# Performance work log

Hardware: AMD Instinct MI355X
Metric: run time of the kernel (lower is better)

Reference implementation:

```python
import jax, jax.numpy as jnp
import numpy as np

N_NODES = 50000
D_IN = 64
HID = 64
OUT = 64
NEG_SLOPE = 0.2


def setup_inputs() -> dict:
    key = jax.random.key(0)
    ks = jax.random.split(key, 16)
    s = 1.0 / np.sqrt(D_IN)
    inp = {
        "x": jax.random.normal(ks[0], (N_NODES, D_IN), dtype=jnp.float32),
        "edge_index": jax.random.randint(ks[1], (2, 1200000), 0, N_NODES, dtype=jnp.int64),
        # conv1 (GATConv, heads=1): separate src/dst projections + attention vectors + bias
        "W1_src": jax.random.uniform(ks[2], (D_IN, HID), jnp.float32, -s, s),
        "W1_dst": jax.random.uniform(ks[3], (D_IN, HID), jnp.float32, -s, s),
        "att1_src": jax.random.uniform(ks[4], (HID,), jnp.float32, -s, s),
        "att1_dst": jax.random.uniform(ks[5], (HID,), jnp.float32, -s, s),
        "b1": jnp.zeros((HID,), jnp.float32),
        # lin1 residual
        "Wl1": jax.random.uniform(ks[6], (D_IN, HID), jnp.float32, -s, s),
        "bl1": jnp.zeros((HID,), jnp.float32),
        # conv2
        "W2_src": jax.random.uniform(ks[7], (HID, OUT), jnp.float32, -s, s),
        "W2_dst": jax.random.uniform(ks[8], (HID, OUT), jnp.float32, -s, s),
        "att2_src": jax.random.uniform(ks[9], (OUT,), jnp.float32, -s, s),
        "att2_dst": jax.random.uniform(ks[10], (OUT,), jnp.float32, -s, s),
        "b2": jnp.zeros((OUT,), jnp.float32),
        # lin2 residual
        "Wl2": jax.random.uniform(ks[11], (HID, OUT), jnp.float32, -s, s),
        "bl2": jnp.zeros((OUT,), jnp.float32),
    }
    return inp


def _gat_conv(x, W_src, W_dst, att_src, att_dst, bias, src, dst, n_nodes):
    # project nodes: [N, C]
    h_src = x @ W_src
    h_dst = x @ W_dst
    # per-node attention logits: [N]
    a_src = h_src @ att_src
    a_dst = h_dst @ att_dst
    # per-edge score, leaky relu (slope 0.2)
    e = a_src[src] + a_dst[dst]  # [E]
    e = jnp.where(e >= 0, e, NEG_SLOPE * e)
    # segment softmax over incoming edges of each dst node
    seg_max = jax.lax.stop_gradient(
        jax.ops.segment_max(e, dst, num_segments=n_nodes))  # [N]
    w = jnp.exp(e - seg_max[dst])  # [E]
    seg_sum = jax.ops.segment_sum(w, dst, num_segments=n_nodes)  # [N]
    alpha = w / seg_sum[dst]  # [E]
    # weighted scatter-add of gathered src features
    msg = h_src[src] * alpha[:, None]  # [E, C]
    out = jax.ops.segment_sum(msg, dst, num_segments=n_nodes)  # [N, C]
    return out + bias


def reference(x, edge_index, W1_src, W1_dst, att1_src, att1_dst, b1, Wl1, bl1,
              W2_src, W2_dst, att2_src, att2_dst, b2, Wl2, bl2):
    src, dst = edge_index[0], edge_index[1]
    n = x.shape[0]
    h = _gat_conv(x, W1_src, W1_dst, att1_src, att1_dst, b1, src, dst, n)
    h = jax.nn.relu(h + x @ Wl1 + bl1)
    o = _gat_conv(h, W2_src, W2_dst, att2_src, att2_dst, b2, src, dst, n)
    o = jax.nn.relu(o + h @ Wl2 + bl2)
    return o
```

## Files before the change

### kernel.cpp

```cpp
#include <hip/hip_runtime.h>
#include <hip/hip_fp16.h>

#define NEG 0.2f
#define BSHIFT 9
#define BNODES 512
#define ECAP 14336

__global__ __launch_bounds__(256) void bin_prep(
    const int* __restrict__ src, const int* __restrict__ dst,
    int* __restrict__ gcur, unsigned* __restrict__ binned, int E, int K,
    const float* __restrict__ W1s, const float* __restrict__ a1s,
    const float* __restrict__ W1d, const float* __restrict__ a1d,
    const float* __restrict__ W2s, const float* __restrict__ a2s,
    const float* __restrict__ W2d, const float* __restrict__ a2d,
    float* __restrict__ vecs) {
    int t = threadIdx.x;
    if (blockIdx.x == gridDim.x - 1) {
        int g = t >> 6, k = t & 63;
        const float* W = (g == 0) ? W1s : (g == 1) ? W1d : (g == 2) ? W2s : W2d;
        const float* a = (g == 0) ? a1s : (g == 1) ? a1d : (g == 2) ? a2s : a2d;
        float s = 0.f;
        #pragma unroll 8
        for (int j = 0; j < 64; ++j) s += W[k * 64 + j] * a[j];
        vecs[t] = s;
        return;
    }
    __shared__ int h[128], cbase[128], cur[128];
    if (t < 128) h[t] = 0;
    __syncthreads();
    int base = blockIdx.x * 2048;
    #pragma unroll
    for (int i = 0; i < 8; ++i) {
        int idx = base + i * 256 + t;
        if (idx < E) atomicAdd(&h[dst[idx] >> BSHIFT], 1);
    }
    __syncthreads();
    if (t < K) {
        cbase[t] = t * ECAP + (h[t] ? atomicAdd(&gcur[t], h[t]) : 0);
        cur[t] = 0;
    }
    __syncthreads();
    #pragma unroll
    for (int i = 0; i < 8; ++i) {
        int idx = base + i * 256 + t;
        if (idx < E) {
            int d = dst[idx], s = src[idx];
            int b = d >> BSHIFT;
            int pos = cbase[b] + atomicAdd(&cur[b], 1);
            binned[pos] = ((unsigned)s << BSHIFT) | (unsigned)(d & (BNODES - 1));
        }
    }
}

__global__ __launch_bounds__(256) void csr_gemm(
    const unsigned* __restrict__ binned, int* __restrict__ ssrc,
    const int* __restrict__ gcur, int* __restrict__ rowbeg, int* __restrict__ rowend,
    const float* __restrict__ x, const float* __restrict__ Wsrc,
    const float* __restrict__ Wl, const float* __restrict__ vsrc,
    const float* __restrict__ vdst, const float* __restrict__ bconv,
    const float* __restrict__ blin,
    __half2* __restrict__ hsrc, float* __restrict__ base_out,
    float* __restrict__ asrc, float* __restrict__ adst, int N, int K) {
    __shared__ union {
        struct { __half WsH[4096]; __half WlH[4096]; float xs[64 * 65];
                 float bias[64]; float vs[64]; float vd[64]; } g;
        struct { int lh[BNODES]; int ps[256]; } c;
    } sm;
    int tid = threadIdx.x;
    int blk = blockIdx.x;

    if (blk < K) {
        int base = blk * ECAP;
        int cnt = min(gcur[blk], ECAP);
        sm.c.lh[tid] = 0; sm.c.lh[tid + 256] = 0;
        __syncthreads();
        for (int i = tid; i < cnt; i += 256)
            atomicAdd(&sm.c.lh[binned[base + i] & (BNODES - 1)], 1);
        __syncthreads();
        int a0 = sm.c.lh[2 * tid], a1 = sm.c.lh[2 * tid + 1];
        sm.c.ps[tid] = a0 + a1;
        __syncthreads();
        for (int off = 1; off < 256; off <<= 1) {
            int v = (tid >= off) ? sm.c.ps[tid - off] : 0;
            __syncthreads();
            sm.c.ps[tid] += v;
            __syncthreads();
        }
        int exc = sm.c.ps[tid] - (a0 + a1);
        int node0 = blk * BNODES + 2 * tid, node1 = node0 + 1;
        if (node0 < N) { rowbeg[node0] = base + exc;      rowend[node0] = base + exc + a0; }
        if (node1 < N) { rowbeg[node1] = base + exc + a0; rowend[node1] = base + exc + a0 + a1; }
        __syncthreads();
        sm.c.lh[2 * tid] = exc; sm.c.lh[2 * tid + 1] = exc + a0;
        __syncthreads();
        for (int i = tid; i < cnt; i += 256) {
            unsigned e = binned[base + i];
            int pos = atomicAdd(&sm.c.lh[e & (BNODES - 1)], 1);
            ssrc[base + pos] = (int)(e >> BSHIFT);
        }
        return;
    }

    int gb = blk - K;
    #pragma unroll
    for (int i = 0; i < 4; ++i) {
        int idx4 = tid * 4 + i * 1024;
        float4 ws = *(const float4*)&Wsrc[idx4];
        float4 wl = *(const float4*)&Wl[idx4];
        *(__half2*)&sm.g.WsH[idx4]     = __floats2half2_rn(ws.x, ws.y);
        *(__half2*)&sm.g.WsH[idx4 + 2] = __floats2half2_rn(ws.z, ws.w);
        *(__half2*)&sm.g.WlH[idx4]     = __floats2half2_rn(wl.x, wl.y);
        *(__half2*)&sm.g.WlH[idx4 + 2] = __floats2half2_rn(wl.z, wl.w);
    }
    if (tid < 64) {
        sm.g.bias[tid] = bconv[tid] + blin[tid];
        sm.g.vs[tid]   = vsrc[tid];
        sm.g.vd[tid]   = vdst[tid];
    }
    int row0 = gb * 64;
    int rows = min(64, N - row0);
    #pragma unroll
    for (int i = 0; i < 16; ++i) {
        int idx = tid + i * 256;
        int r = idx >> 6, cc = idx & 63;
        if (r < rows) sm.g.xs[r * 65 + cc] = x[(size_t)(row0 + r) * 64 + cc];
    }
    __syncthreads();

    int r0 = (tid >> 3) * 2;
    int cg = tid & 7, c0 = cg * 8;
    if (r0 >= rows) return;

    float a0[8], a1[8], b0[8], b1[8];
    #pragma unroll
    for (int i = 0; i < 8; ++i) { a0[i] = a1[i] = b0[i] = b1[i] = 0.f; }
    float as0 = 0.f, ad0 = 0.f, as1 = 0.f, ad1 = 0.f;

    #pragma unroll 8
    for (int k = 0; k < 64; ++k) {
        float xv0 = sm.g.xs[r0 * 65 + k];
        float xv1 = sm.g.xs[(r0 + 1) * 65 + k];
        float4 wsv = *(const float4*)&sm.g.WsH[(k << 6) + c0];
        float4 wlv = *(const float4*)&sm.g.WlH[(k << 6) + c0];
        const __half2* hs = (const __half2*)&wsv;
        const __half2* hl = (const __half2*)&wlv;
        #pragma unroll
        for (int p = 0; p < 4; ++p) {
            float2 w = __half22float2(hs[p]);
            a0[2*p]   += xv0 * w.x;  a0[2*p+1] += xv0 * w.y;
            a1[2*p]   += xv1 * w.x;  a1[2*p+1] += xv1 * w.y;
            float2 l = __half22float2(hl[p]);
            b0[2*p]   += xv0 * l.x;  b0[2*p+1] += xv0 * l.y;
            b1[2*p]   += xv1 * l.x;  b1[2*p+1] += xv1 * l.y;
        }
        float vsk = sm.g.vs[k], vdk = sm.g.vd[k];
        as0 += xv0 * vsk;  ad0 += xv0 * vdk;
        as1 += xv1 * vsk;  ad1 += xv1 * vdk;
    }

    int rg0 = row0 + r0, rg1 = rg0 + 1;
    bool row1ok = (r0 + 1) < rows;
    float4 pack;
    ((__half2*)&pack)[0] = __floats2half2_rn(a0[0], a0[1]);
    ((__half2*)&pack)[1] = __floats2half2_rn(a0[2], a0[3]);
    ((__half2*)&pack)[2] = __floats2half2_rn(a0[4], a0[5]);
    ((__half2*)&pack)[3] = __floats2half2_rn(a0[6], a0[7]);
    *(float4*)&hsrc[(size_t)rg0 * 32 + (c0 >> 1)] = pack;
    if (row1ok) {
        ((__half2*)&pack)[0] = __floats2half2_rn(a1[0], a1[1]);
        ((__half2*)&pack)[1] = __floats2half2_rn(a1[2], a1[3]);
        ((__half2*)&pack)[2] = __floats2half2_rn(a1[4], a1[5]);
        ((__half2*)&pack)[3] = __floats2half2_rn(a1[6], a1[7]);
        *(float4*)&hsrc[(size_t)rg1 * 32 + (c0 >> 1)] = pack;
    }
    float4 bA = *(const float4*)&sm.g.bias[c0];
    float4 bB = *(const float4*)&sm.g.bias[c0 + 4];
    float4 o;
    o.x = b0[0] + bA.x; o.y = b0[1] + bA.y; o.z = b0[2] + bA.z; o.w = b0[3] + bA.w;
    *(float4*)&base_out[(size_t)rg0 * 64 + c0] = o;
    o.x = b0[4] + bB.x; o.y = b0[5] + bB.y; o.z = b0[6] + bB.z; o.w = b0[7] + bB.w;
    *(float4*)&base_out[(size_t)rg0 * 64 + c0 + 4] = o;
    if (row1ok) {
        o.x = b1[0] + bA.x; o.y = b1[1] + bA.y; o.z = b1[2] + bA.z; o.w = b1[3] + bA.w;
        *(float4*)&base_out[(size_t)rg1 * 64 + c0] = o;
        o.x = b1[4] + bB.x; o.y = b1[5] + bB.y; o.z = b1[6] + bB.z; o.w = b1[7] + bB.w;
        *(float4*)&base_out[(size_t)rg1 * 64 + c0 + 4] = o;
    }
    if (cg == 0) {
        asrc[rg0] = as0; adst[rg0] = ad0;
        if (row1ok) { asrc[rg1] = as1; adst[rg1] = ad1; }
    }
}

__global__ __launch_bounds__(256) void node_gemm(
    const float* __restrict__ x, const float* __restrict__ Wsrc,
    const float* __restrict__ Wl, const float* __restrict__ vsrc,
    const float* __restrict__ vdst, const float* __restrict__ bconv,
    const float* __restrict__ blin,
    __half2* __restrict__ hsrc, float* __restrict__ base_out,
    float* __restrict__ asrc, float* __restrict__ adst, int n) {
    __shared__ __half WsH[4096];
    __shared__ __half WlH[4096];
    __shared__ float xs[64 * 65];
    __shared__ float bias_s[64], vs_s[64], vd_s[64];

    int tid = threadIdx.x;
    #pragma unroll
    for (int i = 0; i < 4; ++i) {
        int idx4 = tid * 4 + i * 1024;
        float4 ws = *(const float4*)&Wsrc[idx4];
        float4 wl = *(const float4*)&Wl[idx4];
        *(__half2*)&WsH[idx4]     = __floats2half2_rn(ws.x, ws.y);
        *(__half2*)&WsH[idx4 + 2] = __floats2half2_rn(ws.z, ws.w);
        *(__half2*)&WlH[idx4]     = __floats2half2_rn(wl.x, wl.y);
        *(__half2*)&WlH[idx4 + 2] = __floats2half2_rn(wl.z, wl.w);
    }
    if (tid < 64) {
        bias_s[tid] = bconv[tid] + blin[tid];
        vs_s[tid]   = vsrc[tid];
        vd_s[tid]   = vdst[tid];
    }
    int row0 = blockIdx.x * 64;
    int rows = min(64, n - row0);
    #pragma unroll
    for (int i = 0; i < 16; ++i) {
        int idx = tid + i * 256;
        int r = idx >> 6, cc = idx & 63;
        if (r < rows) xs[r * 65 + cc] = x[(size_t)(row0 + r) * 64 + cc];
    }
    __syncthreads();

    int r0 = (tid >> 3) * 2;
    int cg = tid & 7, c0 = cg * 8;
    if (r0 >= rows) return;

    float a0[8], a1[8], b0[8], b1[8];
    #pragma unroll
    for (int i = 0; i < 8; ++i) { a0[i] = a1[i] = b0[i] = b1[i] = 0.f; }
    float as0 = 0.f, ad0 = 0.f, as1 = 0.f, ad1 = 0.f;

    #pragma unroll 8
    for (int k = 0; k < 64; ++k) {
        float xv0 = xs[r0 * 65 + k];
        float xv1 = xs[(r0 + 1) * 65 + k];
        float4 wsv = *(const float4*)&WsH[(k << 6) + c0];
        float4 wlv = *(const float4*)&WlH[(k << 6) + c0];
        const __half2* hs = (const __half2*)&wsv;
        const __half2* hl = (const __half2*)&wlv;
        #pragma unroll
        for (int p = 0; p < 4; ++p) {
            float2 w = __half22float2(hs[p]);
            a0[2*p]   += xv0 * w.x;  a0[2*p+1] += xv0 * w.y;
            a1[2*p]   += xv1 * w.x;  a1[2*p+1] += xv1 * w.y;
            float2 l = __half22float2(hl[p]);
            b0[2*p]   += xv0 * l.x;  b0[2*p+1] += xv0 * l.y;
            b1[2*p]   += xv1 * l.x;  b1[2*p+1] += xv1 * l.y;
        }
        float vsk = vs_s[k], vdk = vd_s[k];
        as0 += xv0 * vsk;  ad0 += xv0 * vdk;
        as1 += xv1 * vsk;  ad1 += xv1 * vdk;
    }

    int rg0 = row0 + r0, rg1 = rg0 + 1;
    bool row1ok = (r0 + 1) < rows;
    float4 pack;
    ((__half2*)&pack)[0] = __floats2half2_rn(a0[0], a0[1]);
    ((__half2*)&pack)[1] = __floats2half2_rn(a0[2], a0[3]);
    ((__half2*)&pack)[2] = __floats2half2_rn(a0[4], a0[5]);
    ((__half2*)&pack)[3] = __floats2half2_rn(a0[6], a0[7]);
    *(float4*)&hsrc[(size_t)rg0 * 32 + (c0 >> 1)] = pack;
    if (row1ok) {
        ((__half2*)&pack)[0] = __floats2half2_rn(a1[0], a1[1]);
        ((__half2*)&pack)[1] = __floats2half2_rn(a1[2], a1[3]);
        ((__half2*)&pack)[2] = __floats2half2_rn(a1[4], a1[5]);
        ((__half2*)&pack)[3] = __floats2half2_rn(a1[6], a1[7]);
        *(float4*)&hsrc[(size_t)rg1 * 32 + (c0 >> 1)] = pack;
    }
    float4 bA = *(const float4*)&bias_s[c0];
    float4 bB = *(const float4*)&bias_s[c0 + 4];
    float4 o;
    o.x = b0[0] + bA.x; o.y = b0[1] + bA.y; o.z = b0[2] + bA.z; o.w = b0[3] + bA.w;
    *(float4*)&base_out[(size_t)rg0 * 64 + c0] = o;
    o.x = b0[4] + bB.x; o.y = b0[5] + bB.y; o.z = b0[6] + bB.z; o.w = b0[7] + bB.w;
    *(float4*)&base_out[(size_t)rg0 * 64 + c0 + 4] = o;
    if (row1ok) {
        o.x = b1[0] + bA.x; o.y = b1[1] + bA.y; o.z = b1[2] + bA.z; o.w = b1[3] + bA.w;
        *(float4*)&base_out[(size_t)rg1 * 64 + c0] = o;
        o.x = b1[4] + bB.x; o.y = b1[5] + bB.y; o.z = b1[6] + bB.z; o.w = b1[7] + bB.w;
        *(float4*)&base_out[(size_t)rg1 * 64 + c0 + 4] = o;
    }
    if (cg == 0) {
        asrc[rg0] = as0; adst[rg0] = ad0;
        if (row1ok) { asrc[rg1] = as1; adst[rg1] = ad1; }
    }
}

__global__ __launch_bounds__(256) void gat_aggregate(
    const int* __restrict__ rowbeg, const int* __restrict__ rowend,
    const int* __restrict__ ssrc,
    const float* __restrict__ asrc, const float* __restrict__ adst,
    const __half2* __restrict__ hsrc, const float* __restrict__ base,
    float* __restrict__ out, int N) {
    int d = blockIdx.x * 4 + (threadIdx.x >> 6);
    int lane = threadIdx.x & 63;
    int half_id = lane >> 5;
    int c2 = lane & 31;
    if (d >= N) return;
    int beg = rowbeg[d], end = rowend[d];
    float ad = adst[d];
    float sumw = 0.f, accx = 0.f, accy = 0.f;

    while (beg < end) {
        int nb = min(64, end - beg);
        int s_l = 0; float w_l = 0.f;
        if (lane < nb) {
            s_l = ssrc[beg + lane];
            float e = asrc[s_l] + ad;
            e = (e >= 0.f) ? e : NEG * e;
            w_l = __expf(e);
        }
        int i = 0;
        for (; i + 7 < nb; i += 8) {
            int i0 = i + half_id, i1 = i + 2 + half_id;
            int i2 = i + 4 + half_id, i3 = i + 6 + half_id;
            int   s0 = __shfl(s_l, i0, 64), s1 = __shfl(s_l, i1, 64);
            int   s2 = __shfl(s_l, i2, 64), s3 = __shfl(s_l, i3, 64);
            float w0 = __shfl(w_l, i0, 64), w1 = __shfl(w_l, i1, 64);
            float w2 = __shfl(w_l, i2, 64), w3 = __shfl(w_l, i3, 64);
            float2 h0 = __half22float2(hsrc[(size_t)s0 * 32 + c2]);
            float2 h1 = __half22float2(hsrc[(size_t)s1 * 32 + c2]);
            float2 h2 = __half22float2(hsrc[(size_t)s2 * 32 + c2]);
            float2 h3 = __half22float2(hsrc[(size_t)s3 * 32 + c2]);
            sumw += (w0 + w1) + (w2 + w3);
            accx += w0 * h0.x + w1 * h1.x + w2 * h2.x + w3 * h3.x;
            accy += w0 * h0.y + w1 * h1.y + w2 * h2.y + w3 * h3.y;
        }
        for (; i + 3 < nb; i += 4) {
            int i0 = i + half_id, i1 = i + 2 + half_id;
            int   s0 = __shfl(s_l, i0, 64), s1 = __shfl(s_l, i1, 64);
            float w0 = __shfl(w_l, i0, 64), w1 = __shfl(w_l, i1, 64);
            float2 h0 = __half22float2(hsrc[(size_t)s0 * 32 + c2]);
            float2 h1 = __half22float2(hsrc[(size_t)s1 * 32 + c2]);
            sumw += w0 + w1;
            accx += w0 * h0.x + w1 * h1.x;
            accy += w0 * h0.y + w1 * h1.y;
        }
        for (; i < nb; i += 2) {
            int idx = i + half_id;
            int   s = __shfl(s_l, idx, 64);
            float w = __shfl(w_l, idx, 64);
            float2 h = __half22float2(hsrc[(size_t)s * 32 + c2]);
            sumw += w;
            accx += w * h.x;
            accy += w * h.y;
        }
        beg += nb;
    }
    accx += __shfl_xor(accx, 32, 64);
    accy += __shfl_xor(accy, 32, 64);
    sumw += __shfl_xor(sumw, 32, 64);

    if (half_id == 0) {
        float2 b2 = *(const float2*)&base[(size_t)d * 64 + 2 * c2];
        float invw = (sumw > 0.f) ? 1.f / sumw : 0.f;
        float2 o;
        o.x = fmaxf(b2.x + accx * invw, 0.f);
        o.y = fmaxf(b2.y + accy * invw, 0.f);
        *(float2*)&out[(size_t)d * 64 + 2 * c2] = o;
    }
}

extern "C" void kernel_launch(void* const* d_in, const int* in_sizes, int n_in,
                              void* d_out, int out_size, void* d_ws, size_t ws_size,
                              hipStream_t stream) {
    const float* x    = (const float*)d_in[0];
    const int*   ei   = (const int*)d_in[1];
    const float* W1s  = (const float*)d_in[2];
    const float* W1d  = (const float*)d_in[3];
    const float* a1s  = (const float*)d_in[4];
    const float* a1d  = (const float*)d_in[5];
    const float* b1   = (const float*)d_in[6];
    const float* Wl1  = (const float*)d_in[7];
    const float* bl1  = (const float*)d_in[8];
    const float* W2s  = (const float*)d_in[9];
    const float* W2d  = (const float*)d_in[10];
    const float* a2s  = (const float*)d_in[11];
    const float* a2d  = (const float*)d_in[12];
    const float* b2   = (const float*)d_in[13];
    const float* Wl2  = (const float*)d_in[14];
    const float* bl2  = (const float*)d_in[15];

    const int N = in_sizes[0] / 64;
    const int E = in_sizes[1] / 2;
    const int* src = ei;
    const int* dst = ei + E;
    const int K = (N + BNODES - 1) >> BSHIFT;

    float* ws = (float*)d_ws;
    size_t o = 0;
    __half2* hsrcH = (__half2*)(ws + o); o += (size_t)N * 32;
    float* base   = ws + o; o += (size_t)N * 64;
    float* asrc   = ws + o; o += N;
    float* adst   = ws + o; o += N;
    float* vecs   = ws + o; o += 256;
    int* rowbeg = (int*)(ws + o); o += N;
    int* rowend = (int*)(ws + o); o += N;
    int* gcur   = (int*)(ws + o); o += 128;
    unsigned* binned = (unsigned*)(ws + o); o += (size_t)K * ECAP;
    int* ssrc   = (int*)(ws + o); o += (size_t)K * ECAP;

    float* hmid = (float*)d_out;

    const int EB = (E + 2047) / 2048;

    hipMemsetAsync(gcur, 0, 128 * sizeof(int), stream);
    bin_prep<<<EB + 1, 256, 0, stream>>>(src, dst, gcur, binned, E, K,
                                         W1s, a1s, W1d, a1d, W2s, a2s, W2d, a2d, vecs);

    csr_gemm<<<K + (N + 63) / 64, 256, 0, stream>>>(
        binned, ssrc, gcur, rowbeg, rowend,
        x, W1s, Wl1, vecs, vecs + 64, b1, bl1,
        hsrcH, base, asrc, adst, N, K);

    gat_aggregate<<<(N + 3) / 4, 256, 0, stream>>>(rowbeg, rowend, ssrc, asrc, adst,
                                                   hsrcH, base, hmid, N);

    node_gemm<<<(N + 63) / 64, 256, 0, stream>>>(hmid, W2s, Wl2, vecs + 128, vecs + 192,
                                                 b2, bl2, hsrcH, base, asrc, adst, N);
    gat_aggregate<<<(N + 3) / 4, 256, 0, stream>>>(rowbeg, rowend, ssrc, asrc, adst,
                                                   hsrcH, base, (float*)d_out, N);
}
```

Baseline: 240.0 us.

## Fuse layer-1 aggregation into layer-2 GEMM and widen aggregation gathers

Adds an agg_gemm kernel in which each block aggregates 64 destination nodes of layer 1 directly into shared memory, then runs the layer-2 projection GEMM on that tile. This removes the hmid round trip through global memory and one kernel launch. Separate hsrc and asrc/adst buffers per layer keep layer-2 writes from clobbering layer-1 inputs that other blocks still read. Aggregation is reorganised so 16 lanes each gather 8 bytes, handling 4 edges per step instead of 2. The trade-off is less parallelism in the fused aggregation, since each wave walks 16 nodes in sequence and the larger shared-memory footprint may lower occupancy.

```diff
diff --git a/kernel.cpp b/kernel.cpp
--- a/kernel.cpp
+++ b/kernel.cpp
@@ -5,6 +5,58 @@
 #define BSHIFT 9
 #define BNODES 512
 #define ECAP 14336
+
+__device__ __forceinline__ void agg_core(
+    int beg, int end, float ad, int lane, int g, int l,
+    const int* __restrict__ ssrc, const float* __restrict__ asrc,
+    const float2* __restrict__ h8,
+    float& a0, float& a1, float& a2, float& a3, float& sumw) {
+    a0 = a1 = a2 = a3 = sumw = 0.f;
+    while (beg < end) {
+        int nb = min(64, end - beg);
+        int s_l = 0; float w_l = 0.f;
+        if (lane < nb) {
+            s_l = ssrc[beg + lane];
+            float e = asrc[s_l] + ad;
+            e = (e >= 0.f) ? e : NEG * e;
+            w_l = __expf(e);
+        }
+        int i = 0;
+        for (; i + 7 < nb; i += 8) {
+            int iA = i + g, iB = i + 4 + g;
+            int   sA = __shfl(s_l, iA, 64), sB = __shfl(s_l, iB, 64);
+            float wA = __shfl(w_l, iA, 64), wB = __shfl(w_l, iB, 64);
+            float2 rA = h8[(size_t)sA * 16 + l];
+            float2 rB = h8[(size_t)sB * 16 + l];
+            float2 fA0 = __half22float2(((const __half2*)&rA)[0]);
+            float2 fA1 = __half22float2(((const __half2*)&rA)[1]);
+            float2 fB0 = __half22float2(((const __half2*)&rB)[0]);
+            float2 fB1 = __half22float2(((const __half2*)&rB)[1]);
+            sumw += wA + wB;
+            a0 += wA * fA0.x + wB * fB0.x;
+            a1 += wA * fA0.y + wB * fB0.y;
+            a2 += wA * fA1.x + wB * fB1.x;
+            a3 += wA * fA1.y + wB * fB1.y;
+        }
+        for (; i < nb; i += 4) {
+            int iA = i + g;
+            int   sA = __shfl(s_l, iA, 64);
+            float wA = __shfl(w_l, iA, 64);
+            float2 rA = h8[(size_t)sA * 16 + l];
+            float2 fA0 = __half22float2(((const __half2*)&rA)[0]);
+            float2 fA1 = __half22float2(((const __half2*)&rA)[1]);
+            sumw += wA;
+            a0 += wA * fA0.x; a1 += wA * fA0.y;
+            a2 += wA * fA1.x; a3 += wA * fA1.y;
+        }
+        beg += nb;
+    }
+    a0 += __shfl_xor(a0, 16, 64); a0 += __shfl_xor(a0, 32, 64);
+    a1 += __shfl_xor(a1, 16, 64); a1 += __shfl_xor(a1, 32, 64);
+    a2 += __shfl_xor(a2, 16, 64); a2 += __shfl_xor(a2, 32, 64);
+    a3 += __shfl_xor(a3, 16, 64); a3 += __shfl_xor(a3, 32, 64);
+    sumw += __shfl_xor(sumw, 16, 64); sumw += __shfl_xor(sumw, 32, 64);
+}
 
 __global__ __launch_bounds__(256) void bin_prep(
     const int* __restrict__ src, const int* __restrict__ dst,
@@ -52,6 +104,77 @@
     }
 }
 
+__device__ __forceinline__ void gemm_tile(
+    int tid, int row0, int rows,
+    const __half* WsH, const __half* WlH, const float* xs,
+    const float* bias_s, const float* vs_s, const float* vd_s,
+    __half2* __restrict__ hsrc, float* __restrict__ base_out,
+    float* __restrict__ asrc, float* __restrict__ adst) {
+    int r0 = (tid >> 3) * 2;
+    int cg = tid & 7, c0 = cg * 8;
+    if (r0 >= rows) return;
+
+    float a0[8], a1[8], b0[8], b1[8];
+    #pragma unroll
+    for (int i = 0; i < 8; ++i) { a0[i] = a1[i] = b0[i] = b1[i] = 0.f; }
+    float as0 = 0.f, ad0 = 0.f, as1 = 0.f, ad1 = 0.f;
+
+    #pragma unroll 8
+    for (int k = 0; k < 64; ++k) {
+        float xv0 = xs[r0 * 65 + k];
+        float xv1 = xs[(r0 + 1) * 65 + k];
+        float4 wsv = *(const float4*)&WsH[(k << 6) + c0];
+        float4 wlv = *(const float4*)&WlH[(k << 6) + c0];
+        const __half2* hs = (const __half2*)&wsv;
+        const __half2* hl = (const __half2*)&wlv;
+        #pragma unroll
+        for (int p = 0; p < 4; ++p) {
+            float2 w = __half22float2(hs[p]);
+            a0[2*p]   += xv0 * w.x;  a0[2*p+1] += xv0 * w.y;
+            a1[2*p]   += xv1 * w.x;  a1[2*p+1] += xv1 * w.y;
+            float2 l = __half22float2(hl[p]);
+            b0[2*p]   += xv0 * l.x;  b0[2*p+1] += xv0 * l.y;
+            b1[2*p]   += xv1 * l.x;  b1[2*p+1] += xv1 * l.y;
+        }
+        float vsk = vs_s[k], vdk = vd_s[k];
+        as0 += xv0 * vsk;  ad0 += xv0 * vdk;
+        as1 += xv1 * vsk;  ad1 += xv1 * vdk;
+    }
+
+    int rg0 = row0 + r0, rg1 = rg0 + 1;
+    bool row1ok = (r0 + 1) < rows;
+    float4 pack;
+    ((__half2*)&pack)[0] = __floats2half2_rn(a0[0], a0[1]);
+    ((__half2*)&pack)[1] = __floats2half2_rn(a0[2], a0[3]);
+    ((__half2*)&pack)[2] = __floats2half2_rn(a0[4], a0[5]);
+    ((__half2*)&pack)[3] = __floats2half2_rn(a0[6], a0[7]);
+    *(float4*)&hsrc[(size_t)rg0 * 32 + (c0 >> 1)] = pack;
+    if (row1ok) {
+        ((__half2*)&pack)[0] = __floats2half2_rn(a1[0], a1[1]);
+        ((__half2*)&pack)[1] = __floats2half2_rn(a1[2], a1[3]);
+        ((__half2*)&pack)[2] = __floats2half2_rn(a1[4], a1[5]);
+        ((__half2*)&pack)[3] = __floats2half2_rn(a1[6], a1[7]);
+        *(float4*)&hsrc[(size_t)rg1 * 32 + (c0 >> 1)] = pack;
+    }
+    float4 bA = *(const float4*)&bias_s[c0];
+    float4 bB = *(const float4*)&bias_s[c0 + 4];
+    float4 o;
+    o.x = b0[0] + bA.x; o.y = b0[1] + bA.y; o.z = b0[2] + bA.z; o.w = b0[3] + bA.w;
+    *(float4*)&base_out[(size_t)rg0 * 64 + c0] = o;
+    o.x = b0[4] + bB.x; o.y = b0[5] + bB.y; o.z = b0[6] + bB.z; o.w = b0[7] + bB.w;
+    *(float4*)&base_out[(size_t)rg0 * 64 + c0 + 4] = o;
+    if (row1ok) {
+        o.x = b1[0] + bA.x; o.y = b1[1] + bA.y; o.z = b1[2] + bA.z; o.w = b1[3] + bA.w;
+        *(float4*)&base_out[(size_t)rg1 * 64 + c0] = o;
+        o.x = b1[4] + bB.x; o.y = b1[5] + bB.y; o.z = b1[6] + bB.z; o.w = b1[7] + bB.w;
+        *(float4*)&base_out[(size_t)rg1 * 64 + c0 + 4] = o;
+    }
+    if (cg == 0) {
+        asrc[rg0] = as0; adst[rg0] = ad0;
+        if (row1ok) { asrc[rg1] = as1; adst[rg1] = ad1; }
+    }
+}
+
 __global__ __launch_bounds__(256) void csr_gemm(
     const unsigned* __restrict__ binned, int* __restrict__ ssrc,
     const int* __restrict__ gcur, int* __restrict__ rowbeg, int* __restrict__ rowend,
@@ -126,79 +249,20 @@
         if (r < rows) sm.g.xs[r * 65 + cc] = x[(size_t)(row0 + r) * 64 + cc];
     }
     __syncthreads();
-
-    int r0 = (tid >> 3) * 2;
-    int cg = tid & 7, c0 = cg * 8;
-    if (r0 >= rows) return;
-
-    float a0[8], a1[8], b0[8], b1[8];
-    #pragma unroll
-    for (int i = 0; i < 8; ++i) { a0[i] = a1[i] = b0[i] = b1[i] = 0.f; }
-    float as0 = 0.f, ad0 = 0.f, as1 = 0.f, ad1 = 0.f;
-
-    #pragma unroll 8
-    for (int k = 0; k < 64; ++k) {
-        float xv0 = sm.g.xs[r0 * 65 + k];
-        float xv1 = sm.g.xs[(r0 + 1) * 65 + k];
-        float4 wsv = *(const float4*)&sm.g.WsH[(k << 6) + c0];
-        float4 wlv = *(const float4*)&sm.g.WlH[(k << 6) + c0];
-        const __half2* hs = (const __half2*)&wsv;
-        const __half2* hl = (const __half2*)&wlv;
-        #pragma unroll
-        for (int p = 0; p < 4; ++p) {
-            float2 w = __half22float2(hs[p]);
-            a0[2*p]   += xv0 * w.x;  a0[2*p+1] += xv0 * w.y;
-            a1[2*p]   += xv1 * w.x;  a1[2*p+1] += xv1 * w.y;
-            float2 l = __half22float2(hl[p]);
-            b0[2*p]   += xv0 * l.x;  b0[2*p+1] += xv0 * l.y;
-            b1[2*p]   += xv1 * l.x;  b1[2*p+1] += xv1 * l.y;
-        }
-        float vsk = sm.g.vs[k], vdk = sm.g.vd[k];
-        as0 += xv0 * vsk;  ad0 += xv0 * vdk;
-        as1 += xv1 * vsk;  ad1 += xv1 * vdk;
-    }
-
-    int rg0 = row0 + r0, rg1 = rg0 + 1;
-    bool row1ok = (r0 + 1) < rows;
-    float4 pack;
-    ((__half2*)&pack)[0] = __floats2half2_rn(a0[0], a0[1]);
-    ((__half2*)&pack)[1] = __floats2half2_rn(a0[2], a0[3]);
-    ((__half2*)&pack)[2] = __floats2half2_rn(a0[4], a0[5]);
-    ((__half2*)&pack)[3] = __floats2half2_rn(a0[6], a0[7]);
-    *(float4*)&hsrc[(size_t)rg0 * 32 + (c0 >> 1)] = pack;
-    if (row1ok) {
-        ((__half2*)&pack)[0] = __floats2half2_rn(a1[0], a1[1]);
-        ((__half2*)&pack)[1] = __floats2half2_rn(a1[2], a1[3]);
-        ((__half2*)&pack)[2] = __floats2half2_rn(a1[4], a1[5]);
-        ((__half2*)&pack)[3] = __floats2half2_rn(a1[6], a1[7]);
-        *(float4*)&hsrc[(size_t)rg1 * 32 + (c0 >> 1)] = pack;
-    }
-    float4 bA = *(const float4*)&sm.g.bias[c0];
-    float4 bB = *(const float4*)&sm.g.bias[c0 + 4];
-    float4 o;
-    o.x = b0[0] + bA.x; o.y = b0[1] + bA.y; o.z = b0[2] + bA.z; o.w = b0[3] + bA.w;
-    *(float4*)&base_out[(size_t)rg0 * 64 + c0] = o;
-    o.x = b0[4] + bB.x; o.y = b0[5] + bB.y; o.z = b0[6] + bB.z; o.w = b0[7] + bB.w;
-    *(float4*)&base_out[(size_t)rg0 * 64 + c0 + 4] = o;
-    if (row1ok) {
-        o.x = b1[0] + bA.x; o.y = b1[1] + bA.y; o.z = b1[2] + bA.z; o.w = b1[3] + bA.w;
-        *(float4*)&base_out[(size_t)rg1 * 64 + c0] = o;
-        o.x = b1[4] + bB.x; o.y = b1[5] + bB.y; o.z = b1[6] + bB.z; o.w = b1[7] + bB.w;
-        *(float4*)&base_out[(size_t)rg1 * 64 + c0 + 4] = o;
-    }
-    if (cg == 0) {
-        asrc[rg0] = as0; adst[rg0] = ad0;
-        if (row1ok) { asrc[rg1] = as1; adst[rg1] = ad1; }
-    }
-}
-
-__global__ __launch_bounds__(256) void node_gemm(
-    const float* __restrict__ x, const float* __restrict__ Wsrc,
-    const float* __restrict__ Wl, const float* __restrict__ vsrc,
-    const float* __restrict__ vdst, const float* __restrict__ bconv,
-    const float* __restrict__ blin,
-    __half2* __restrict__ hsrc, float* __restrict__ base_out,
-    float* __restrict__ asrc, float* __restrict__ adst, int n) {
+    gemm_tile(tid, row0, rows, sm.g.WsH, sm.g.WlH, sm.g.xs,
+              sm.g.bias, sm.g.vs, sm.g.vd, hsrc, base_out, asrc, adst);
+}
+
+__global__ __launch_bounds__(256) void agg_gemm(
+    const int* __restrict__ rowbeg, const int* __restrict__ rowend,
+    const int* __restrict__ ssrc,
+    const float* __restrict__ asrc1, const float* __restrict__ adst1,
+    const float2* __restrict__ h8_1, const float* __restrict__ base1,
+    const float* __restrict__ Wsrc, const float* __restrict__ Wl,
+    const float* __restrict__ vsrc, const float* __restrict__ vdst,
+    const float* __restrict__ bconv, const float* __restrict__ blin,
+    __half2* __restrict__ hsrc2, float* __restrict__ base2,
+    float* __restrict__ asrc2, float* __restrict__ adst2, int N) {
     __shared__ __half WsH[4096];
     __shared__ __half WlH[4096];
     __shared__ float xs[64 * 65];
@@ -220,153 +284,55 @@
         vs_s[tid]   = vsrc[tid];
         vd_s[tid]   = vdst[tid];
     }
+
     int row0 = blockIdx.x * 64;
-    int rows = min(64, n - row0);
-    #pragma unroll
-    for (int i = 0; i < 16; ++i) {
-        int idx = tid + i * 256;
-        int r = idx >> 6, cc = idx & 63;
-        if (r < rows) xs[r * 65 + cc] = x[(size_t)(row0 + r) * 64 + cc];
+    int rows = min(64, N - row0);
+    int wave = tid >> 6, lane = tid & 63, g = lane >> 4, l = lane & 15;
+    #pragma unroll 1
+    for (int k = 0; k < 16; ++k) {
+        int d = row0 + wave * 16 + k;
+        if (d < N) {
+            float a0, a1, a2, a3, sw;
+            agg_core(rowbeg[d], rowend[d], adst1[d], lane, g, l,
+                     ssrc, asrc1, h8_1, a0, a1, a2, a3, sw);
+            if (g == 0) {
+                float4 b4 = *(const float4*)&base1[(size_t)d * 64 + 4 * l];
+                float invw = (sw > 0.f) ? 1.f / sw : 0.f;
+                float4 r;
+                r.x = fmaxf(b4.x + a0 * invw, 0.f);
+                r.y = fmaxf(b4.y + a1 * invw, 0.f);
+                r.z = fmaxf(b4.z + a2 * invw, 0.f);
+                r.w = fmaxf(b4.w + a3 * invw, 0.f);
+                *(float4*)&xs[(d - row0) * 65 + 4 * l] = r;
+            }
+        }
     }
     __syncthreads();
-
-    int r0 = (tid >> 3) * 2;
-    int cg = tid & 7, c0 = cg * 8;
-    if (r0 >= rows) return;
-
-    float a0[8], a1[8], b0[8], b1[8];
-    #pragma unroll
-    for (int i = 0; i < 8; ++i) { a0[i] = a1[i] = b0[i] = b1[i] = 0.f; }
-    float as0 = 0.f, ad0 = 0.f, as1 = 0.f, ad1 = 0.f;
-
-    #pragma unroll 8
-    for (int k = 0; k < 64; ++k) {
-        float xv0 = xs[r0 * 65 + k];
-        float xv1 = xs[(r0 + 1) * 65 + k];
-        float4 wsv = *(const float4*)&WsH[(k << 6) + c0];
-        float4 wlv = *(const float4*)&WlH[(k << 6) + c0];
-        const __half2* hs = (const __half2*)&wsv;
-        const __half2* hl = (const __half2*)&wlv;
-        #pragma unroll
-        for (int p = 0; p < 4; ++p) {
-            float2 w = __half22float2(hs[p]);
-            a0[2*p]   += xv0 * w.x;  a0[2*p+1] += xv0 * w.y;
-            a1[2*p]   += xv1 * w.x;  a1[2*p+1] += xv1 * w.y;
-            float2 l = __half22float2(hl[p]);
-            b0[2*p]   += xv0 * l.x;  b0[2*p+1] += xv0 * l.y;
-            b1[2*p]   += xv1 * l.x;  b1[2*p+1] += xv1 * l.y;
-        }
-        float vsk = vs_s[k], vdk = vd_s[k];
-        as0 += xv0 * vsk;  ad0 += xv0 * vdk;
-        as1 += xv1 * vsk;  ad1 += xv1 * vdk;
-    }
-
-    int rg0 = row0 + r0, rg1 = rg0 + 1;
-    bool row1ok = (r0 + 1) < rows;
-    float4 pack;
-    ((__half2*)&pack)[0] = __floats2half2_rn(a0[0], a0[1]);
-    ((__half2*)&pack)[1] = __floats2half2_rn(a0[2], a0[3]);
-    ((__half2*)&pack)[2] = __floats2half2_rn(a0[4], a0[5]);
-    ((__half2*)&pack)[3] = __floats2half2_rn(a0[6], a0[7]);
-    *(float4*)&hsrc[(size_t)rg0 * 32 + (c0 >> 1)] = pack;
-    if (row1ok) {
-        ((__half2*)&pack)[0] = __floats2half2_rn(a1[0], a1[1]);
-        ((__half2*)&pack)[1] = __floats2half2_rn(a1[2], a1[3]);
-        ((__half2*)&pack)[2] = __floats2half2_rn(a1[4], a1[5]);
-        ((__half2*)&pack)[3] = __floats2half2_rn(a1[6], a1[7]);
-        *(float4*)&hsrc[(size_t)rg1 * 32 + (c0 >> 1)] = pack;
-    }
-    float4 bA = *(const float4*)&bias_s[c0];
-    float4 bB = *(const float4*)&bias_s[c0 + 4];
-    float4 o;
-    o.x = b0[0] + bA.x; o.y = b0[1] + bA.y; o.z = b0[2] + bA.z; o.w = b0[3] + bA.w;
-    *(float4*)&base_out[(size_t)rg0 * 64 + c0] = o;
-    o.x = b0[4] + bB.x; o.y = b0[5] + bB.y; o.z = b0[6] + bB.z; o.w = b0[7] + bB.w;
-    *(float4*)&base_out[(size_t)rg0 * 64 + c0 + 4] = o;
-    if (row1ok) {
-        o.x = b1[0] + bA.x; o.y = b1[1] + bA.y; o.z = b1[2] + bA.z; o.w = b1[3] + bA.w;
-        *(float4*)&base_out[(size_t)rg1 * 64 + c0] = o;
-        o.x = b1[4] + bB.x; o.y = b1[5] + bB.y; o.z = b1[6] + bB.z; o.w = b1[7] + bB.w;
-        *(float4*)&base_out[(size_t)rg1 * 64 + c0 + 4] = o;
-    }
-    if (cg == 0) {
-        asrc[rg0] = as0; adst[rg0] = ad0;
-        if (row1ok) { asrc[rg1] = as1; adst[rg1] = ad1; }
-    }
+    gemm_tile(tid, row0, rows, WsH, WlH, xs, bias_s, vs_s, vd_s,
+              hsrc2, base2, asrc2, adst2);
 }
 
 __global__ __launch_bounds__(256) void gat_aggregate(
     const int* __restrict__ rowbeg, const int* __restrict__ rowend,
     const int* __restrict__ ssrc,
     const float* __restrict__ asrc, const float* __restrict__ adst,
-    const __half2* __restrict__ hsrc, const float* __restrict__ base,
+    const float2* __restrict__ h8, const float* __restrict__ base,
     float* __restrict__ out, int N) {
     int d = blockIdx.x * 4 + (threadIdx.x >> 6);
-    int lane = threadIdx.x & 63;
-    int half_id = lane >> 5;
-    int c2 = lane & 31;
+    int lane = threadIdx.x & 63, g = lane >> 4, l = lane & 15;
     if (d >= N) return;
-    int beg = rowbeg[d], end = rowend[d];
-    float ad = adst[d];
-    float sumw = 0.f, accx = 0.f, accy = 0.f;
-
-    while (beg < end) {
-        int nb = min(64, end - beg);
-        int s_l = 0; float w_l = 0.f;
-        if (lane < nb) {
-            s_l = ssrc[beg + lane];
-            float e = asrc[s_l] + ad;
-            e = (e >= 0.f) ? e : NEG * e;
-            w_l = __expf(e);
-        }
-        int i = 0;
-        for (; i + 7 < nb; i += 8) {
-            int i0 = i + half_id, i1 = i + 2 + half_id;
-            int i2 = i + 4 + half_id, i3 = i + 6 + half_id;
-            int   s0 = __shfl(s_l, i0, 64), s1 = __shfl(s_l, i1, 64);
-            int   s2 = __shfl(s_l, i2, 64), s3 = __shfl(s_l, i3, 64);
-            float w0 = __shfl(w_l, i0, 64), w1 = __shfl(w_l, i1, 64);
-            float w2 = __shfl(w_l, i2, 64), w3 = __shfl(w_l, i3, 64);
-            float2 h0 = __half22float2(hsrc[(size_t)s0 * 32 + c2]);
-            float2 h1 = __half22float2(hsrc[(size_t)s1 * 32 + c2]);
-            float2 h2 = __half22float2(hsrc[(size_t)s2 * 32 + c2]);
-            float2 h3 = __half22float2(hsrc[(size_t)s3 * 32 + c2]);
-            sumw += (w0 + w1) + (w2 + w3);
-            accx += w0 * h0.x + w1 * h1.x + w2 * h2.x + w3 * h3.x;
-            accy += w0 * h0.y + w1 * h1.y + w2 * h2.y + w3 * h3.y;
-        }
-        for (; i + 3 < nb; i += 4) {
-            int i0 = i + half_id, i1 = i + 2 + half_id;
-            int   s0 = __shfl(s_l, i0, 64), s1 = __shfl(s_l, i1, 64);
-            float w0 = __shfl(w_l, i0, 64), w1 = __shfl(w_l, i1, 64);
-            float2 h0 = __half22float2(hsrc[(size_t)s0 * 32 + c2]);
-            float2 h1 = __half22float2(hsrc[(size_t)s1 * 32 + c2]);
-            sumw += w0 + w1;
-            accx += w0 * h0.x + w1 * h1.x;
-            accy += w0 * h0.y + w1 * h1.y;
-        }
-        for (; i < nb; i += 2) {
-            int idx = i + half_id;
-            int   s = __shfl(s_l, idx, 64);
-            float w = __shfl(w_l, idx, 64);
-            float2 h = __half22float2(hsrc[(size_t)s * 32 + c2]);
-            sumw += w;
-            accx += w * h.x;
-            accy += w * h.y;
-        }
-        beg += nb;
-    }
-    accx += __shfl_xor(accx, 32, 64);
-    accy += __shfl_xor(accy, 32, 64);
-    sumw += __shfl_xor(sumw, 32, 64);
-
-    if (half_id == 0) {
-        float2 b2 = *(const float2*)&base[(size_t)d * 64 + 2 * c2];
-        float invw = (sumw > 0.f) ? 1.f / sumw : 0.f;
-        float2 o;
-        o.x = fmaxf(b2.x + accx * invw, 0.f);
-        o.y = fmaxf(b2.y + accy * invw, 0.f);
-        *(float2*)&out[(size_t)d * 64 + 2 * c2] = o;
+    float a0, a1, a2, a3, sw;
+    agg_core(rowbeg[d], rowend[d], adst[d], lane, g, l, ssrc, asrc, h8,
+             a0, a1, a2, a3, sw);
+    if (g == 0) {
+        float4 b4 = *(const float4*)&base[(size_t)d * 64 + 4 * l];
+        float invw = (sw > 0.f) ? 1.f / sw : 0.f;
+        float4 o;
+        o.x = fmaxf(b4.x + a0 * invw, 0.f);
+        o.y = fmaxf(b4.y + a1 * invw, 0.f);
+        o.z = fmaxf(b4.z + a2 * invw, 0.f);
+        o.w = fmaxf(b4.w + a3 * invw, 0.f);
+        *(float4*)&out[(size_t)d * 64 + 4 * l] = o;
     }
 }
 
@@ -398,10 +364,13 @@
 
     float* ws = (float*)d_ws;
     size_t o = 0;
-    __half2* hsrcH = (__half2*)(ws + o); o += (size_t)N * 32;
+    __half2* hsrc1 = (__half2*)(ws + o); o += (size_t)N * 32;
+    __half2* hsrc2 = (__half2*)(ws + o); o += (size_t)N * 32;
     float* base   = ws + o; o += (size_t)N * 64;
-    float* asrc   = ws + o; o += N;
-    float* adst   = ws + o; o += N;
+    float* asrc1  = ws + o; o += N;
+    float* adst1  = ws + o; o += N;
+    float* asrc2  = ws + o; o += N;
+    float* adst2  = ws + o; o += N;
     float* vecs   = ws + o; o += 256;
     int* rowbeg = (int*)(ws + o); o += N;
     int* rowend = (int*)(ws + o); o += N;
@@ -409,24 +378,24 @@
     unsigned* binned = (unsigned*)(ws + o); o += (size_t)K * ECAP;
     int* ssrc   = (int*)(ws + o); o += (size_t)K * ECAP;
 
-    float* hmid = (float*)d_out;
-
     const int EB = (E + 2047) / 2048;
+    const int GB = (N + 63) / 64;
 
     hipMemsetAsync(gcur, 0, 128 * sizeof(int), stream);
     bin_prep<<<EB + 1, 256, 0, stream>>>(src, dst, gcur, binned, E, K,
                                          W1s, a1s, W1d, a1d, W2s, a2s, W2d, a2d, vecs);
 
-    csr_gemm<<<K + (N + 63) / 64, 256, 0, stream>>>(
+    csr_gemm<<<K + GB, 256, 0, stream>>>(
         binned, ssrc, gcur, rowbeg, rowend,
         x, W1s, Wl1, vecs, vecs + 64, b1, bl1,
-        hsrcH, base, asrc, adst, N, K);
-
-    gat_aggregate<<<(N + 3) / 4, 256, 0, stream>>>(rowbeg, rowend, ssrc, asrc, adst,
-                                                   hsrcH, base, hmid, N);
-
-    node_gemm<<<(N + 63) / 64, 256, 0, stream>>>(hmid, W2s, Wl2, vecs + 128, vecs + 192,
-                                                 b2, bl2, hsrcH, base, asrc, adst, N);
-    gat_aggregate<<<(N + 3) / 4, 256, 0, stream>>>(rowbeg, rowend, ssrc, asrc, adst,
-                                                   hsrcH, base, (float*)d_out, N);
-}
+        hsrc1, base, asrc1, adst1, N, K);
+
+    agg_gemm<<<GB, 256, 0, stream>>>(
+        rowbeg, rowend, ssrc, asrc1, adst1, (const float2*)hsrc1, base,
+        W2s, Wl2, vecs + 128, vecs + 192, b2, bl2,
+        hsrc2, base, asrc2, adst2, N);
+
+    gat_aggregate<<<(N + 3) / 4, 256, 0, stream>>>(
+        rowbeg, rowend, ssrc, asrc2, adst2, (const float2*)hsrc2, base,
+        (float*)d_out, N);
+}
```

Result: slower. 247.7 us (+3.2%).
